# Kernel tuning notes

Hardware: AMD Instinct MI355X
Metric: run time of the kernel (lower is better)

The kernel has to match this reference:

```python
import jax, jax.numpy as jnp
import numpy as np

N, HID, NH = 4096, 1024, 8
D = HID // NH            # ret_size = 128
F_SCALE = 1.0
GAMMA = 1.0 - 2.0 ** (-5)
SCALE_EXP = D ** (-0.5)
LN_EPS = 1e-5


def setup_inputs() -> dict:
    key = jax.random.key(0)
    ks = jax.random.split(key, 12)
    s = HID ** (-0.5)
    return {
        "cur_hiddens": jax.random.normal(ks[0], (N, HID), jnp.float32),
        "f_adj": jax.random.uniform(ks[1], (N, N), jnp.float32),
        "f_dist": jax.random.uniform(ks[2], (N, N), jnp.float32),
        "f_clb": jax.random.normal(ks[3], (N, N), jnp.float32),
        "Wq": jax.random.normal(ks[4], (HID, HID), jnp.float32) * s,
        "Wk": jax.random.normal(ks[5], (HID, HID), jnp.float32) * s,
        "Wv": jax.random.normal(ks[6], (HID, HID), jnp.float32) * s,
        "Wo": jax.random.normal(ks[7], (HID, HID), jnp.float32) * s,
        "bo": jax.random.normal(ks[8], (HID,), jnp.float32) * 0.01,
        "ln_g": jnp.ones((HID,), jnp.float32),
        "ln_b": jnp.zeros((HID,), jnp.float32),
    }


def _layer_norm(x, g, b):
    mu = jnp.mean(x, axis=-1, keepdims=True)
    var = jnp.mean(jnp.square(x - mu), axis=-1, keepdims=True)
    return (x - mu) * jax.lax.rsqrt(var + LN_EPS) * g + b


def reference(cur_hiddens, f_adj, f_dist, f_clb, Wq, Wk, Wv, Wo, bo, ln_g, ln_b):
    n = cur_hiddens.shape[0]
    # projections, reshaped to (heads, atoms, ret_size)
    q = (cur_hiddens @ Wq).reshape(n, NH, D).transpose(1, 0, 2)
    k = (cur_hiddens @ Wk).reshape(n, NH, D).transpose(1, 0, 2)
    v = (cur_hiddens @ Wv).reshape(n, NH, D).transpose(1, 0, 2)
    # retention scores per head: (NH, n, n)
    scores = jnp.einsum('hnd,hmd->hnm', q, k)
    # per-head structural bias injection (no softmax on scores)
    adj_b = F_SCALE * f_adj
    dist_b = F_SCALE * jax.nn.softmax(f_dist, axis=1)
    clb_b = F_SCALE * jax.nn.softmax(f_clb, axis=1)
    scores = scores.at[0].add(adj_b).at[1].add(adj_b)
    scores = scores.at[2].add(dist_b).at[3].add(dist_b)
    scores = scores.at[4].add(clb_b).at[5].add(clb_b)
    scores = scores * (GAMMA ** SCALE_EXP)
    # retention output
    ret = jnp.einsum('hnm,hmd->hnd', scores, v)
    ret = jax.nn.relu(ret)                          # act_func (dropout p=0)
    ret = ret.transpose(1, 0, 2).reshape(n, HID)    # (n, NH*D)
    out = ret @ Wo + bo
    mol_vec = _layer_norm(cur_hiddens + out, ln_g, ln_b)
    return mol_vec, jnp.mean(scores, axis=0)
```

## Files before the change

kernel.cpp:

```cpp
#include <hip/hip_runtime.h>
#include <math.h>

#define NA     4096
#define HID    1024
#define LN_EPS 1e-5f

typedef short s8   __attribute__((ext_vector_type(8)));
typedef float f32x4 __attribute__((ext_vector_type(4)));

#define OFF_XBF   ((size_t)0)
#define OFF_WQT   ((size_t)8<<20)
#define OFF_WKT   ((size_t)10<<20)
#define OFF_WVT   ((size_t)12<<20)
#define OFF_QB    ((size_t)14<<20)
#define OFF_KB    ((size_t)22<<20)
#define OFF_VB    ((size_t)30<<20)
#define OFF_KT    ((size_t)38<<20)
#define OFF_VT    ((size_t)46<<20)
#define OFF_WOT   ((size_t)54<<20)
#define OFF_M2F   ((size_t)56<<20)
#define OFF_M2B   (OFF_M2F + ((size_t)512<<10))
#define OFF_RMAXD (OFF_M2F + ((size_t)768<<10))
#define OFF_RINVD (OFF_RMAXD + 16384)
#define OFF_RMAXC (OFF_RINVD + 16384)
#define OFF_RINVC (OFF_RMAXC + 16384)
#define OFF_RETF  ((size_t)22<<20)
#define OFF_RETB  ((size_t)34<<20)
#define OFF_YF    ((size_t)0)

__device__ __forceinline__ ushort f2bf(float f) {
    unsigned u = __float_as_uint(f);
    u += 0x7FFFu + ((u >> 16) & 1u);
    return (ushort)(u >> 16);
}

__device__ __forceinline__ void gl16(const void* g, void* l) {
    __builtin_amdgcn_global_load_lds(
        (const __attribute__((address_space(1))) void*)g,
        (__attribute__((address_space(3))) void*)l, 16, 0, 0);
}

__device__ __forceinline__ void mfma_tile(const short* As, const short* Bs,
                                          f32x4 (&acc)[4][4], int lane, int wr, int wc)
{
    const int r = lane & 15, kg = (lane >> 4) * 8;
    s8 a[4], b[4];
#pragma unroll
    for (int i = 0; i < 4; i++) a[i] = *(const s8*)&As[(wr*64 + i*16 + r)*32 + kg];
#pragma unroll
    for (int j = 0; j < 4; j++) b[j] = *(const s8*)&Bs[(wc*64 + j*16 + r)*32 + kg];
#pragma unroll
    for (int i = 0; i < 4; i++)
#pragma unroll
        for (int j = 0; j < 4; j++)
            acc[i][j] = __builtin_amdgcn_mfma_f32_16x16x32_bf16(a[i], b[j], acc[i][j], 0, 0, 0);
}

__device__ __forceinline__ void gemm_bf16_nt_async(const ushort* A, int lda,
    const ushort* Bt, int ldb, int K, int row0, int col0,
    short* As, short* Bs, f32x4 (&acc)[4][4], int tid)
{
    const int lane = tid & 63, wave = tid >> 6, wr = wave >> 1, wc = wave & 1;
    const int srow = wave*32 + (lane >> 2), scol = (lane & 3) * 8;
    const ushort* Ap0 = A  + (size_t)(row0 + srow) * lda + scol;
    const ushort* Ap1 = Ap0 + 16 * (size_t)lda;
    const ushort* Bp0 = Bt + (size_t)(col0 + srow) * ldb + scol;
    const ushort* Bp1 = Bp0 + 16 * (size_t)ldb;
    short* As0 = As + (wave*32)*32;
    short* As1 = As + (wave*32+16)*32;
    short* Bs0 = Bs + (wave*32)*32;
    short* Bs1 = Bs + (wave*32+16)*32;
    for (int kt = 0; kt < K; kt += 32) {
        __syncthreads();
        gl16(Ap0 + kt, As0);
        gl16(Ap1 + kt, As1);
        gl16(Bp0 + kt, Bs0);
        gl16(Bp1 + kt, Bs1);
        __syncthreads();
        mfma_tile(As, Bs, acc, lane, wr, wc);
    }
}

#define ZERO_ACC(acc) { f32x4 z = {0.f,0.f,0.f,0.f}; \
    _Pragma("unroll") for (int i=0;i<4;i++) _Pragma("unroll") for (int j=0;j<4;j++) acc[i][j]=z; }

__global__ __launch_bounds__(256) void k_prep(const float* __restrict__ X,
    const float* __restrict__ Wq, const float* __restrict__ Wk,
    const float* __restrict__ Wv, const float* __restrict__ Wo, char* __restrict__ wsb)
{
    const int z = blockIdx.z, bx = blockIdx.x, by = blockIdx.y, t = threadIdx.x;
    const int lr = t >> 2, jb = t & 3;
    if (z == 0) {
        const float* src = X + (size_t)(by*64 + lr) * HID + bx*64 + jb*16;
        ushort* dst = (ushort*)(wsb + OFF_XBF) + (size_t)(by*64 + lr) * HID + bx*64 + jb*16;
        union { ushort u[16]; uint4 q[2]; } pk;
        union { float f[16]; float4 v[4]; } fa;
#pragma unroll
        for (int m = 0; m < 4; m++) fa.v[m] = ((const float4*)src)[m];
#pragma unroll
        for (int m = 0; m < 16; m++) pk.u[m] = f2bf(fa.f[m]);
        ((uint4*)dst)[0] = pk.q[0]; ((uint4*)dst)[1] = pk.q[1];
        return;
    }
    if (by >= 16) return;
    __shared__ ushort Tl[64][72];
    const float* W = (z == 1) ? Wq : (z == 2) ? Wk : (z == 3) ? Wv : Wo;
    ushort* WT = (ushort*)(wsb + ((z==1)?OFF_WQT:(z==2)?OFF_WKT:(z==3)?OFF_WVT:OFF_WOT));
    const int r0 = by*64, c0 = bx*64;
    const float* src = W + (size_t)(r0 + lr) * HID + c0 + jb*16;
    union { float f[16]; float4 v[4]; } fa;
#pragma unroll
    for (int m = 0; m < 4; m++) fa.v[m] = ((const float4*)src)[m];
#pragma unroll
    for (int m = 0; m < 16; m++) Tl[lr][jb*16 + m] = f2bf(fa.f[m]);
    __syncthreads();
    union { ushort u[16]; uint4 q[2]; } pk;
#pragma unroll
    for (int m = 0; m < 16; m++) pk.u[m] = Tl[jb*16 + m][lr];
    ushort* dst = WT + (size_t)(c0 + lr) * HID + r0 + jb*16;
    ((uint4*)dst)[0] = pk.q[0]; ((uint4*)dst)[1] = pk.q[1];
}

__global__ __launch_bounds__(256) void k_rowstats(const float* __restrict__ f_dist,
    const float* __restrict__ f_clb, char* __restrict__ wsb)
{
    const int row = blockIdx.x, mat = blockIdx.y, t = threadIdx.x;
    const float* F = mat ? f_clb : f_dist;
    float* rmax = (float*)(wsb + (mat ? OFF_RMAXC : OFF_RMAXD));
    float* rinv = (float*)(wsb + (mat ? OFF_RINVC : OFF_RINVD));
    float4 v[4];
#pragma unroll
    for (int p = 0; p < 4; p++)
        v[p] = *(const float4*)(F + (size_t)row * NA + 4*t + 1024*p);
    float m = -1e30f;
#pragma unroll
    for (int p = 0; p < 4; p++)
        m = fmaxf(m, fmaxf(fmaxf(v[p].x, v[p].y), fmaxf(v[p].z, v[p].w)));
    for (int off = 32; off; off >>= 1) m = fmaxf(m, __shfl_xor(m, off));
    __shared__ float sb[4];
    if ((t & 63) == 0) sb[t >> 6] = m;
    __syncthreads();
    const float m4 = fmaxf(fmaxf(sb[0], sb[1]), fmaxf(sb[2], sb[3]));
    __syncthreads();
    float s = 0.f;
#pragma unroll
    for (int p = 0; p < 4; p++)
        s += expf(v[p].x-m4) + expf(v[p].y-m4) + expf(v[p].z-m4) + expf(v[p].w-m4);
    for (int off = 32; off; off >>= 1) s += __shfl_xor(s, off);
    if ((t & 63) == 0) sb[t >> 6] = s;
    __syncthreads();
    if (t == 0) { rmax[row] = m4; rinv[row] = 1.0f / (sb[0]+sb[1]+sb[2]+sb[3]); }
}

__global__ __launch_bounds__(256) void k_proj(char* __restrict__ wsb)
{
    __shared__ __align__(16) short As[128*32], Bs[128*32];
    const int z = blockIdx.z;
    const ushort* A  = (const ushort*)(wsb + OFF_XBF);
    const ushort* Bt = (const ushort*)(wsb + ((z==0)?OFF_WQT:(z==1)?OFF_WKT:OFF_WVT));
    ushort* O = (ushort*)(wsb + ((z==0)?OFF_QB:(z==1)?OFF_KB:OFF_VB));
    const int row0 = blockIdx.y*128, col0 = blockIdx.x*128;
    f32x4 acc[4][4]; ZERO_ACC(acc);
    gemm_bf16_nt_async(A, HID, Bt, HID, HID, row0, col0, As, Bs, acc, threadIdx.x);
    const int lane = threadIdx.x & 63, wave = threadIdx.x >> 6, wr = wave>>1, wc = wave&1;
#pragma unroll
    for (int i = 0; i < 4; i++)
#pragma unroll
    for (int e = 0; e < 4; e++) {
        const int r = row0 + wr*64 + i*16 + (lane>>4)*4 + e;
#pragma unroll
        for (int j = 0; j < 4; j++) {
            const int c = col0 + wc*64 + j*16 + (lane & 15);
            O[(size_t)r*HID + c] = f2bf(acc[i][j][e]);
        }
    }
}

__global__ __launch_bounds__(256) void k_transKV(char* __restrict__ wsb)
{
    const int z = blockIdx.z;
    const ushort* in = (const ushort*)(wsb + (z ? OFF_VB : OFF_KB));
    ushort* out = (ushort*)(wsb + (z ? OFF_VT : OFF_KT));
    const int n0 = blockIdx.y*64, c0 = blockIdx.x*64;
    const int t = threadIdx.x, lr = t >> 2, jb = t & 3;
    __shared__ ushort Tl[64][72];
    const ushort* src = in + (size_t)(n0 + lr) * HID + c0 + jb*16;
    union { ushort u[16]; uint4 q[2]; } pk;
    pk.q[0] = ((const uint4*)src)[0]; pk.q[1] = ((const uint4*)src)[1];
#pragma unroll
    for (int m = 0; m < 16; m++) Tl[lr][jb*16 + m] = pk.u[m];
    __syncthreads();
#pragma unroll
    for (int m = 0; m < 16; m++) pk.u[m] = Tl[jb*16 + m][lr];
    ushort* dst = out + (size_t)(c0 + lr) * NA + n0 + jb*16;
    ((uint4*)dst)[0] = pk.q[0]; ((uint4*)dst)[1] = pk.q[1];
}

__global__ __launch_bounds__(256) void k_ktv(char* __restrict__ wsb)
{
    __shared__ __align__(16) short As[128*32], Bs[128*32];
    const int ci = blockIdx.x, h = blockIdx.y;
    const ushort* A  = (const ushort*)(wsb + OFF_VT) + (size_t)h*128*NA + ci*256;
    const ushort* Bt = (const ushort*)(wsb + OFF_KT) + (size_t)h*128*NA + ci*256;
    f32x4 acc[4][4]; ZERO_ACC(acc);
    gemm_bf16_nt_async(A, NA, Bt, NA, 256, 0, 0, As, Bs, acc, threadIdx.x);
    float* M2f = (float*)(wsb + OFF_M2F) + (size_t)h*16384;
    const int lane = threadIdx.x & 63, wave = threadIdx.x >> 6, wr = wave>>1, wc = wave&1;
#pragma unroll
    for (int i = 0; i < 4; i++)
#pragma unroll
    for (int e = 0; e < 4; e++) {
        const int r = wr*64 + i*16 + (lane>>4)*4 + e;
#pragma unroll
        for (int j = 0; j < 4; j++) {
            const int c = wc*64 + j*16 + (lane & 15);
            atomicAdd(&M2f[r*128 + c], acc[i][j][e]);
        }
    }
}

__global__ __launch_bounds__(256) void k_m2cvt(char* __restrict__ wsb)
{
    const int i = (blockIdx.x*256 + threadIdx.x) * 8;
    const float* s = (const float*)(wsb + OFF_M2F);
    ushort* d = (ushort*)(wsb + OFF_M2B);
    union { float f[8]; float4 v[2]; } fa;
    fa.v[0] = *(const float4*)(s + i); fa.v[1] = *(const float4*)(s + i + 4);
    union { ushort u[8]; uint4 q; } pk;
#pragma unroll
    for (int m = 0; m < 8; m++) pk.u[m] = f2bf(fa.f[m]);
    *(uint4*)(d + i) = pk.q;
}

__global__ __launch_bounds__(256) void k_scores(char* __restrict__ wsb,
    const float* __restrict__ f_adj, const float* __restrict__ f_dist,
    const float* __restrict__ f_clb, float* __restrict__ outs, float cdiv8, float cdiv4)
{
    __shared__ __align__(16) short As[128*32], Bs[128*32];
    const int lin = blockIdx.y*32 + blockIdx.x;
    const int sw  = (lin & 7)*128 + (lin >> 3);
    const int row0 = (sw >> 5)*128, col0 = (sw & 31)*128;
    f32x4 acc[4][4]; ZERO_ACC(acc);
    gemm_bf16_nt_async((const ushort*)(wsb + OFF_QB), HID,
                       (const ushort*)(wsb + OFF_KB), HID, HID, row0, col0,
                       As, Bs, acc, threadIdx.x);
    const float* rmaxd = (const float*)(wsb + OFF_RMAXD);
    const float* rinvd = (const float*)(wsb + OFF_RINVD);
    const float* rmaxc = (const float*)(wsb + OFF_RMAXC);
    const float* rinvc = (const float*)(wsb + OFF_RINVC);
    const int lane = threadIdx.x & 63, wave = threadIdx.x >> 6, wr = wave>>1, wc = wave&1;
#pragma unroll
    for (int i = 0; i < 4; i++)
#pragma unroll
    for (int e = 0; e < 4; e++) {
        const int r = row0 + wr*64 + i*16 + (lane>>4)*4 + e;
        const float rmd = rmaxd[r], rid = rinvd[r], rmc = rmaxc[r], ric = rinvc[r];
#pragma unroll
        for (int j = 0; j < 4; j++) {
            const int c = col0 + wc*64 + j*16 + (lane & 15);
            const size_t idx = (size_t)r * NA + c;
            const float bias = f_adj[idx] + __expf(f_dist[idx]-rmd)*rid
                                          + __expf(f_clb[idx]-rmc)*ric;
            outs[idx] = cdiv8 * acc[i][j][e] + cdiv4 * bias;
        }
    }
}

__global__ __launch_bounds__(512, 2) void k_ret2(char* __restrict__ wsb,
    const float* __restrict__ f_adj, const float* __restrict__ f_dist,
    const float* __restrict__ f_clb)
{
    __shared__ __align__(16) short As[128*32];
    __shared__ __align__(16) short Bs[256*32];
    const int kc = blockIdx.x;
    const int row0 = blockIdx.y * 128;
    const int p = blockIdx.z;
    const int tid = threadIdx.x, lane = tid & 63, wave = tid >> 6;
    const int wr = wave >> 2, wc = wave & 3;
    const int ar = tid >> 2, ac = (tid & 3) * 8;
    const int srow = wave*32 + (lane >> 2), scol = (lane & 3) * 8;

    const float* F = (p == 0) ? f_adj : (p == 1) ? f_dist : f_clb;
    float rm = 0.f, ri = 1.f;
    if (p) {
        rm = ((const float*)(wsb + ((p==1) ? OFF_RMAXD : OFF_RMAXC)))[row0 + ar];
        ri = ((const float*)(wsb + ((p==1) ? OFF_RINVD : OFF_RINVC)))[row0 + ar];
    }
    const float*  Fp  = F + (size_t)(row0 + ar) * NA + kc*1024 + ac;
    const ushort* Bp0 = (const ushort*)(wsb + OFF_VT) + (size_t)(p*256 + srow) * NA + kc*1024 + scol;
    const ushort* Bp1 = Bp0 + 16 * (size_t)NA;
    short* Ad  = &As[ar * 32 + ac];
    short* Bs0 = &Bs[(wave*32)*32];
    short* Bs1 = &Bs[(wave*32+16)*32];

    f32x4 acc[4][4]; ZERO_ACC(acc);
    for (int kt = 0; kt < 1024; kt += 32) {
        union { float f[8]; float4 v[2]; } fa;
        fa.v[0] = *(const float4*)(Fp + kt);
        fa.v[1] = *(const float4*)(Fp + kt + 4);
        if (p) {
#pragma unroll
            for (int m = 0; m < 8; m++) fa.f[m] = __expf(fa.f[m] - rm) * ri;
        }
        union { ushort u[8]; uint4 q; } pk;
#pragma unroll
        for (int m = 0; m < 8; m++) pk.u[m] = f2bf(fa.f[m]);
        __syncthreads();
        gl16(Bp0 + kt, Bs0);
        gl16(Bp1 + kt, Bs1);
        *(uint4*)Ad = pk.q;
        __syncthreads();
        mfma_tile(As, Bs, acc, lane, wr, wc);
    }
    float* RF = (float*)(wsb + OFF_RETF);
#pragma unroll
    for (int i = 0; i < 4; i++)
#pragma unroll
    for (int e = 0; e < 4; e++) {
        const int r = row0 + wr*64 + i*16 + (lane>>4)*4 + e;
#pragma unroll
        for (int j = 0; j < 4; j++) {
            const int c = p*256 + wc*64 + j*16 + (lane & 15);
            atomicAdd(&RF[(size_t)r * 768 + c], acc[i][j][e]);
        }
    }
}

__global__ __launch_bounds__(256) void k_retfin(char* __restrict__ wsb, float c_scale)
{
    __shared__ __align__(16) short As[128*32], Bs[128*32];
    const int h = blockIdx.x, row0 = blockIdx.y * 128;
    const ushort* A  = (const ushort*)(wsb + OFF_QB) + (size_t)row0 * HID + h*128;
    const ushort* Bt = (const ushort*)(wsb + OFF_M2B) + (size_t)h * 16384;
    f32x4 acc[4][4]; ZERO_ACC(acc);
    gemm_bf16_nt_async(A, HID, Bt, 128, 128, 0, 0, As, Bs, acc, threadIdx.x);
    const float* RF = (const float*)(wsb + OFF_RETF);
    ushort* RB = (ushort*)(wsb + OFF_RETB);
    const int lane = threadIdx.x & 63, wave = threadIdx.x >> 6, wr = wave>>1, wc = wave&1;
#pragma unroll
    for (int i = 0; i < 4; i++)
#pragma unroll
    for (int e = 0; e < 4; e++) {
        const int r = row0 + wr*64 + i*16 + (lane>>4)*4 + e;
#pragma unroll
        for (int j = 0; j < 4; j++) {
            const int cl = wc*64 + j*16 + (lane & 15);
            const int col = h*128 + cl;
            float v = acc[i][j][e];
            if (h < 6) v += RF[(size_t)r * 768 + col];
            RB[(size_t)r * HID + col] = f2bf(fmaxf(c_scale * v, 0.f));
        }
    }
}

__global__ __launch_bounds__(256) void k_wo(char* __restrict__ wsb,
    const float* __restrict__ X, const float* __restrict__ bo)
{
    __shared__ __align__(16) short As[128*32], Bs[128*32];
    const int row0 = blockIdx.y*128, col0 = blockIdx.x*128;
    f32x4 acc[4][4]; ZERO_ACC(acc);
    gemm_bf16_nt_async((const ushort*)(wsb + OFF_RETB), HID,
                       (const ushort*)(wsb + OFF_WOT), HID, HID, row0, col0,
                       As, Bs, acc, threadIdx.x);
    float* Y = (float*)(wsb + OFF_YF);
    const int lane = threadIdx.x & 63, wave = threadIdx.x >> 6, wr = wave>>1, wc = wave&1;
#pragma unroll
    for (int i = 0; i < 4; i++)
#pragma unroll
    for (int e = 0; e < 4; e++) {
        const int r = row0 + wr*64 + i*16 + (lane>>4)*4 + e;
#pragma unroll
        for (int j = 0; j < 4; j++) {
            const int c = col0 + wc*64 + j*16 + (lane & 15);
            Y[(size_t)r*HID + c] = acc[i][j][e] + X[(size_t)r*HID + c] + bo[c];
        }
    }
}

__global__ __launch_bounds__(256) void k_ln(const char* __restrict__ wsb,
    const float* __restrict__ g, const float* __restrict__ b, float* __restrict__ out)
{
    const float* Y = (const float*)(wsb + OFF_YF);
    const int row = blockIdx.x, t = threadIdx.x;
    float4 v = *(const float4*)(Y + (size_t)row * HID + 4*t);
    float s = v.x + v.y + v.z + v.w;
    for (int off = 32; off; off >>= 1) s += __shfl_xor(s, off);
    __shared__ float sb[4];
    if ((t & 63) == 0) sb[t >> 6] = s;
    __syncthreads();
    const float mu = (sb[0]+sb[1]+sb[2]+sb[3]) * (1.0f / HID);
    const float dx = v.x-mu, dy = v.y-mu, dz = v.z-mu, dw = v.w-mu;
    float q = dx*dx + dy*dy + dz*dz + dw*dw;
    __syncthreads();
    for (int off = 32; off; off >>= 1) q += __shfl_xor(q, off);
    if ((t & 63) == 0) sb[t >> 6] = q;
    __syncthreads();
    const float var = (sb[0]+sb[1]+sb[2]+sb[3]) * (1.0f / HID);
    const float rstd = rsqrtf(var + LN_EPS);
    float4 gv = *(const float4*)(g + 4*t);
    float4 bv = *(const float4*)(b + 4*t);
    float4 o = make_float4(dx*rstd*gv.x + bv.x, dy*rstd*gv.y + bv.y,
                           dz*rstd*gv.z + bv.z, dw*rstd*gv.w + bv.w);
    *(float4*)(out + (size_t)row * HID + 4*t) = o;
}

extern "C" void kernel_launch(void* const* d_in, const int* in_sizes, int n_in,
                              void* d_out, int out_size, void* d_ws, size_t ws_size,
                              hipStream_t stream)
{
    const float* X      = (const float*)d_in[0];
    const float* f_adj  = (const float*)d_in[1];
    const float* f_dist = (const float*)d_in[2];
    const float* f_clb  = (const float*)d_in[3];
    const float* Wq     = (const float*)d_in[4];
    const float* Wk     = (const float*)d_in[5];
    const float* Wv     = (const float*)d_in[6];
    const float* Wo     = (const float*)d_in[7];
    const float* bo     = (const float*)d_in[8];
    const float* ln_g   = (const float*)d_in[9];
    const float* ln_b   = (const float*)d_in[10];

    char* wsb = (char*)d_ws;
    float* out = (float*)d_out;
    float* out_scores = out + (size_t)NA * HID;

    const float c_scale = (float)pow(1.0 - 1.0/32.0, 1.0 / sqrt(128.0));

    hipMemsetAsync(wsb + OFF_M2F, 0, (size_t)512 << 10, stream);

    k_prep    <<<dim3(16, 64, 5), 256, 0, stream>>>(X, Wq, Wk, Wv, Wo, wsb);
    k_rowstats<<<dim3(NA, 2),     256, 0, stream>>>(f_dist, f_clb, wsb);
    k_proj    <<<dim3(8, 32, 3),  256, 0, stream>>>(wsb);
    k_transKV <<<dim3(16, 64, 2), 256, 0, stream>>>(wsb);
    k_ktv     <<<dim3(16, 8),     256, 0, stream>>>(wsb);
    k_m2cvt   <<<64,              256, 0, stream>>>(wsb);
    k_scores  <<<dim3(32, 32),    256, 0, stream>>>(wsb, f_adj, f_dist, f_clb,
                                                    out_scores, c_scale/8.f, c_scale/4.f);
    hipMemsetAsync(wsb + OFF_RETF, 0, (size_t)NA * 768 * 4, stream);
    k_ret2    <<<dim3(4, 32, 3),  512, 0, stream>>>(wsb, f_adj, f_dist, f_clb);
    k_retfin  <<<dim3(8, 32),     256, 0, stream>>>(wsb, c_scale);
    k_wo      <<<dim3(8, 32),     256, 0, stream>>>(wsb, X, bo);
    k_ln      <<<NA,              256, 0, stream>>>(wsb, ln_g, ln_b, out);
}
```

Measured before the change: 544.8 us.

## Double-buffer LDS in all GEMMs, compute V transposed directly, drop scores swizzle

```diff
diff --git a/kernel.cpp b/kernel.cpp
--- a/kernel.cpp
+++ b/kernel.cpp
@@ -56,7 +56,7 @@
             acc[i][j] = __builtin_amdgcn_mfma_f32_16x16x32_bf16(a[i], b[j], acc[i][j], 0, 0, 0);
 }
 
-__device__ __forceinline__ void gemm_bf16_nt_async(const ushort* A, int lda,
+__device__ __forceinline__ void gemm_bf16_nt_db(const ushort* A, int lda,
     const ushort* Bt, int ldb, int K, int row0, int col0,
     short* As, short* Bs, f32x4 (&acc)[4][4], int tid)
 {
@@ -66,19 +66,20 @@
     const ushort* Ap1 = Ap0 + 16 * (size_t)lda;
     const ushort* Bp0 = Bt + (size_t)(col0 + srow) * ldb + scol;
     const ushort* Bp1 = Bp0 + 16 * (size_t)ldb;
-    short* As0 = As + (wave*32)*32;
-    short* As1 = As + (wave*32+16)*32;
-    short* Bs0 = Bs + (wave*32)*32;
-    short* Bs1 = Bs + (wave*32+16)*32;
-    for (int kt = 0; kt < K; kt += 32) {
+    const int o0 = (wave*32)*32, o1 = o0 + 512;
+    gl16(Ap0, As + o0); gl16(Ap1, As + o1);
+    gl16(Bp0, Bs + o0); gl16(Bp1, Bs + o1);
+    __syncthreads();
+    int cur = 0;
+    for (int kt = 32; kt < K; kt += 32) {
+        const int nb = (cur ^ 1) * 4096;
+        gl16(Ap0 + kt, As + nb + o0); gl16(Ap1 + kt, As + nb + o1);
+        gl16(Bp0 + kt, Bs + nb + o0); gl16(Bp1 + kt, Bs + nb + o1);
+        mfma_tile(As + cur*4096, Bs + cur*4096, acc, lane, wr, wc);
         __syncthreads();
-        gl16(Ap0 + kt, As0);
-        gl16(Ap1 + kt, As1);
-        gl16(Bp0 + kt, Bs0);
-        gl16(Bp1 + kt, Bs1);
-        __syncthreads();
-        mfma_tile(As, Bs, acc, lane, wr, wc);
-    }
+        cur ^= 1;
+    }
+    mfma_tile(As + cur*4096, Bs + cur*4096, acc, lane, wr, wc);
 }
 
 #define ZERO_ACC(acc) { f32x4 z = {0.f,0.f,0.f,0.f}; \
@@ -154,33 +155,54 @@
 
 __global__ __launch_bounds__(256) void k_proj(char* __restrict__ wsb)
 {
-    __shared__ __align__(16) short As[128*32], Bs[128*32];
+    __shared__ __align__(16) short As[2*4096], Bs[2*4096];
     const int z = blockIdx.z;
-    const ushort* A  = (const ushort*)(wsb + OFF_XBF);
-    const ushort* Bt = (const ushort*)(wsb + ((z==0)?OFF_WQT:(z==1)?OFF_WKT:OFF_WVT));
-    ushort* O = (ushort*)(wsb + ((z==0)?OFF_QB:(z==1)?OFF_KB:OFF_VB));
-    const int row0 = blockIdx.y*128, col0 = blockIdx.x*128;
-    f32x4 acc[4][4]; ZERO_ACC(acc);
-    gemm_bf16_nt_async(A, HID, Bt, HID, HID, row0, col0, As, Bs, acc, threadIdx.x);
+    const ushort* A; const ushort* Bt; int row0, col0;
+    if (z < 2) {
+        A  = (const ushort*)(wsb + OFF_XBF);
+        Bt = (const ushort*)(wsb + (z ? OFF_WKT : OFF_WQT));
+        row0 = blockIdx.y*128; col0 = blockIdx.x*128;
+    } else {
+        A  = (const ushort*)(wsb + OFF_WVT);
+        Bt = (const ushort*)(wsb + OFF_XBF);
+        row0 = blockIdx.x*128; col0 = blockIdx.y*128;
+    }
+    f32x4 acc[4][4]; ZERO_ACC(acc);
+    gemm_bf16_nt_db(A, HID, Bt, HID, HID, row0, col0, As, Bs, acc, threadIdx.x);
     const int lane = threadIdx.x & 63, wave = threadIdx.x >> 6, wr = wave>>1, wc = wave&1;
-#pragma unroll
-    for (int i = 0; i < 4; i++)
-#pragma unroll
-    for (int e = 0; e < 4; e++) {
-        const int r = row0 + wr*64 + i*16 + (lane>>4)*4 + e;
-#pragma unroll
-        for (int j = 0; j < 4; j++) {
-            const int c = col0 + wc*64 + j*16 + (lane & 15);
-            O[(size_t)r*HID + c] = f2bf(acc[i][j][e]);
-        }
-    }
-}
-
-__global__ __launch_bounds__(256) void k_transKV(char* __restrict__ wsb)
-{
-    const int z = blockIdx.z;
-    const ushort* in = (const ushort*)(wsb + (z ? OFF_VB : OFF_KB));
-    ushort* out = (ushort*)(wsb + (z ? OFF_VT : OFF_KT));
+    if (z < 2) {
+        ushort* O = (ushort*)(wsb + (z ? OFF_KB : OFF_QB));
+#pragma unroll
+        for (int i = 0; i < 4; i++)
+#pragma unroll
+        for (int e = 0; e < 4; e++) {
+            const int r = row0 + wr*64 + i*16 + (lane>>4)*4 + e;
+#pragma unroll
+            for (int j = 0; j < 4; j++) {
+                const int c = col0 + wc*64 + j*16 + (lane & 15);
+                O[(size_t)r*HID + c] = f2bf(acc[i][j][e]);
+            }
+        }
+    } else {
+        ushort* VT = (ushort*)(wsb + OFF_VT);
+#pragma unroll
+        for (int i = 0; i < 4; i++)
+#pragma unroll
+        for (int e = 0; e < 4; e++) {
+            const int r = row0 + wr*64 + i*16 + (lane>>4)*4 + e;
+#pragma unroll
+            for (int j = 0; j < 4; j++) {
+                const int c = col0 + wc*64 + j*16 + (lane & 15);
+                VT[(size_t)r*NA + c] = f2bf(acc[i][j][e]);
+            }
+        }
+    }
+}
+
+__global__ __launch_bounds__(256) void k_transK(char* __restrict__ wsb)
+{
+    const ushort* in = (const ushort*)(wsb + OFF_KB);
+    ushort* out = (ushort*)(wsb + OFF_KT);
     const int n0 = blockIdx.y*64, c0 = blockIdx.x*64;
     const int t = threadIdx.x, lr = t >> 2, jb = t & 3;
     __shared__ ushort Tl[64][72];
@@ -198,12 +220,12 @@
 
 __global__ __launch_bounds__(256) void k_ktv(char* __restrict__ wsb)
 {
-    __shared__ __align__(16) short As[128*32], Bs[128*32];
+    __shared__ __align__(16) short As[2*4096], Bs[2*4096];
     const int ci = blockIdx.x, h = blockIdx.y;
     const ushort* A  = (const ushort*)(wsb + OFF_VT) + (size_t)h*128*NA + ci*256;
     const ushort* Bt = (const ushort*)(wsb + OFF_KT) + (size_t)h*128*NA + ci*256;
     f32x4 acc[4][4]; ZERO_ACC(acc);
-    gemm_bf16_nt_async(A, NA, Bt, NA, 256, 0, 0, As, Bs, acc, threadIdx.x);
+    gemm_bf16_nt_db(A, NA, Bt, NA, 256, 0, 0, As, Bs, acc, threadIdx.x);
     float* M2f = (float*)(wsb + OFF_M2F) + (size_t)h*16384;
     const int lane = threadIdx.x & 63, wave = threadIdx.x >> 6, wr = wave>>1, wc = wave&1;
 #pragma unroll
@@ -236,14 +258,12 @@
     const float* __restrict__ f_adj, const float* __restrict__ f_dist,
     const float* __restrict__ f_clb, float* __restrict__ outs, float cdiv8, float cdiv4)
 {
-    __shared__ __align__(16) short As[128*32], Bs[128*32];
-    const int lin = blockIdx.y*32 + blockIdx.x;
-    const int sw  = (lin & 7)*128 + (lin >> 3);
-    const int row0 = (sw >> 5)*128, col0 = (sw & 31)*128;
-    f32x4 acc[4][4]; ZERO_ACC(acc);
-    gemm_bf16_nt_async((const ushort*)(wsb + OFF_QB), HID,
-                       (const ushort*)(wsb + OFF_KB), HID, HID, row0, col0,
-                       As, Bs, acc, threadIdx.x);
+    __shared__ __align__(16) short As[2*4096], Bs[2*4096];
+    const int row0 = blockIdx.y*128, col0 = blockIdx.x*128;
+    f32x4 acc[4][4]; ZERO_ACC(acc);
+    gemm_bf16_nt_db((const ushort*)(wsb + OFF_QB), HID,
+                    (const ushort*)(wsb + OFF_KB), HID, HID, row0, col0,
+                    As, Bs, acc, threadIdx.x);
     const float* rmaxd = (const float*)(wsb + OFF_RMAXD);
     const float* rinvd = (const float*)(wsb + OFF_RINVD);
     const float* rmaxc = (const float*)(wsb + OFF_RMAXC);
@@ -270,8 +290,8 @@
     const float* __restrict__ f_adj, const float* __restrict__ f_dist,
     const float* __restrict__ f_clb)
 {
-    __shared__ __align__(16) short As[128*32];
-    __shared__ __align__(16) short Bs[256*32];
+    __shared__ __align__(16) short As[2*4096];
+    __shared__ __align__(16) short Bs[2*8192];
     const int kc = blockIdx.x;
     const int row0 = blockIdx.y * 128;
     const int p = blockIdx.z;
@@ -289,15 +309,34 @@
     const float*  Fp  = F + (size_t)(row0 + ar) * NA + kc*1024 + ac;
     const ushort* Bp0 = (const ushort*)(wsb + OFF_VT) + (size_t)(p*256 + srow) * NA + kc*1024 + scol;
     const ushort* Bp1 = Bp0 + 16 * (size_t)NA;
-    short* Ad  = &As[ar * 32 + ac];
-    short* Bs0 = &Bs[(wave*32)*32];
-    short* Bs1 = &Bs[(wave*32+16)*32];
-
-    f32x4 acc[4][4]; ZERO_ACC(acc);
-    for (int kt = 0; kt < 1024; kt += 32) {
+    const int bo0 = (wave*32)*32, bo1 = bo0 + 512;
+    const int aoff = ar*32 + ac;
+
+    f32x4 acc[4][4]; ZERO_ACC(acc);
+    {
+        union { float f[8]; float4 v[2]; } fa;
+        fa.v[0] = *(const float4*)(Fp);
+        fa.v[1] = *(const float4*)(Fp + 4);
+        gl16(Bp0, Bs + bo0); gl16(Bp1, Bs + bo1);
+        if (p) {
+#pragma unroll
+            for (int m = 0; m < 8; m++) fa.f[m] = __expf(fa.f[m] - rm) * ri;
+        }
+        union { ushort u[8]; uint4 q; } pk;
+#pragma unroll
+        for (int m = 0; m < 8; m++) pk.u[m] = f2bf(fa.f[m]);
+        *(uint4*)(As + aoff) = pk.q;
+        __syncthreads();
+    }
+    int cur = 0;
+    for (int kt = 32; kt < 1024; kt += 32) {
+        const int nxt = cur ^ 1;
         union { float f[8]; float4 v[2]; } fa;
         fa.v[0] = *(const float4*)(Fp + kt);
         fa.v[1] = *(const float4*)(Fp + kt + 4);
+        gl16(Bp0 + kt, Bs + nxt*8192 + bo0);
+        gl16(Bp1 + kt, Bs + nxt*8192 + bo1);
+        mfma_tile(As + cur*4096, Bs + cur*8192, acc, lane, wr, wc);
         if (p) {
 #pragma unroll
             for (int m = 0; m < 8; m++) fa.f[m] = __expf(fa.f[m] - rm) * ri;
@@ -305,13 +344,12 @@
         union { ushort u[8]; uint4 q; } pk;
 #pragma unroll
         for (int m = 0; m < 8; m++) pk.u[m] = f2bf(fa.f[m]);
+        *(uint4*)(As + nxt*4096 + aoff) = pk.q;
         __syncthreads();
-        gl16(Bp0 + kt, Bs0);
-        gl16(Bp1 + kt, Bs1);
-        *(uint4*)Ad = pk.q;
-        __syncthreads();
-        mfma_tile(As, Bs, acc, lane, wr, wc);
-    }
+        cur = nxt;
+    }
+    mfma_tile(As + cur*4096, Bs + cur*8192, acc, lane, wr, wc);
+
     float* RF = (float*)(wsb + OFF_RETF);
 #pragma unroll
     for (int i = 0; i < 4; i++)
@@ -328,12 +366,12 @@
 
 __global__ __launch_bounds__(256) void k_retfin(char* __restrict__ wsb, float c_scale)
 {
-    __shared__ __align__(16) short As[128*32], Bs[128*32];
+    __shared__ __align__(16) short As[2*4096], Bs[2*4096];
     const int h = blockIdx.x, row0 = blockIdx.y * 128;
     const ushort* A  = (const ushort*)(wsb + OFF_QB) + (size_t)row0 * HID + h*128;
     const ushort* Bt = (const ushort*)(wsb + OFF_M2B) + (size_t)h * 16384;
     f32x4 acc[4][4]; ZERO_ACC(acc);
-    gemm_bf16_nt_async(A, HID, Bt, 128, 128, 0, 0, As, Bs, acc, threadIdx.x);
+    gemm_bf16_nt_db(A, HID, Bt, 128, 128, 0, 0, As, Bs, acc, threadIdx.x);
     const float* RF = (const float*)(wsb + OFF_RETF);
     ushort* RB = (ushort*)(wsb + OFF_RETB);
     const int lane = threadIdx.x & 63, wave = threadIdx.x >> 6, wr = wave>>1, wc = wave&1;
@@ -356,12 +394,12 @@
 __global__ __launch_bounds__(256) void k_wo(char* __restrict__ wsb,
     const float* __restrict__ X, const float* __restrict__ bo)
 {
-    __shared__ __align__(16) short As[128*32], Bs[128*32];
+    __shared__ __align__(16) short As[2*4096], Bs[2*4096];
     const int row0 = blockIdx.y*128, col0 = blockIdx.x*128;
     f32x4 acc[4][4]; ZERO_ACC(acc);
-    gemm_bf16_nt_async((const ushort*)(wsb + OFF_RETB), HID,
-                       (const ushort*)(wsb + OFF_WOT), HID, HID, row0, col0,
-                       As, Bs, acc, threadIdx.x);
+    gemm_bf16_nt_db((const ushort*)(wsb + OFF_RETB), HID,
+                    (const ushort*)(wsb + OFF_WOT), HID, HID, row0, col0,
+                    As, Bs, acc, threadIdx.x);
     float* Y = (float*)(wsb + OFF_YF);
     const int lane = threadIdx.x & 63, wave = threadIdx.x >> 6, wr = wave>>1, wc = wave&1;
 #pragma unroll
@@ -431,7 +469,7 @@
     k_prep    <<<dim3(16, 64, 5), 256, 0, stream>>>(X, Wq, Wk, Wv, Wo, wsb);
     k_rowstats<<<dim3(NA, 2),     256, 0, stream>>>(f_dist, f_clb, wsb);
     k_proj    <<<dim3(8, 32, 3),  256, 0, stream>>>(wsb);
-    k_transKV <<<dim3(16, 64, 2), 256, 0, stream>>>(wsb);
+    k_transK  <<<dim3(16, 64),    256, 0, stream>>>(wsb);
     k_ktv     <<<dim3(16, 8),     256, 0, stream>>>(wsb);
     k_m2cvt   <<<64,              256, 0, stream>>>(wsb);
     k_scores  <<<dim3(32, 32),    256, 0, stream>>>(wsb, f_adj, f_dist, f_clb,
```

After: 548.9 us. About the same (+0.8%).
